# Kernel tuning notes

Hardware: AMD Instinct MI355X
Metric: run time of the kernel (lower is better)

Reference implementation:

```python
import jax, jax.numpy as jnp
import numpy as np

R_CUT = 5.0
N_NODES = 50000
N_EDGES = 400000
N_GRAPHS = 2500
D = 128        # embedding_size (hardcoded by torch.split(..., 128))
N_RBF = 20
N_BLOCKS = 3
PI = 3.141592653589793


def setup_inputs() -> dict:
    key = jax.random.key(0)
    ks = jax.random.split(key, 32)
    w = lambda k, s: (jax.random.normal(k, s) * 0.05).astype(jnp.float32)
    z = jax.random.randint(ks[0], (N_NODES,), 0, 100)
    edges = jax.random.randint(ks[1], (N_EDGES, 2), 0, N_NODES)
    r_ij = jax.random.uniform(ks[2], (N_EDGES, 1), minval=0.8, maxval=R_CUT, dtype=jnp.float32)
    d = jax.random.normal(ks[3], (N_EDGES, 3), dtype=jnp.float32)
    r_ij_normalized = d / jnp.linalg.norm(d, axis=1, keepdims=True)
    graph_idx = jax.random.randint(ks[4], (N_NODES,), 0, N_GRAPHS)
    return {
        "z": z, "edges": edges, "r_ij": r_ij,
        "r_ij_normalized": r_ij_normalized, "graph_idx": graph_idx,
        "emb": w(ks[5], (100, D)),
        # message blocks (stacked over N_BLOCKS)
        "msg_w1": w(ks[6], (N_BLOCKS, D, D)),   "msg_b1": w(ks[7], (N_BLOCKS, D)),
        "msg_w2": w(ks[8], (N_BLOCKS, D, 3 * D)), "msg_b2": w(ks[9], (N_BLOCKS, 3 * D)),
        "rbf_w": w(ks[10], (N_BLOCKS, N_RBF, 3 * D)), "rbf_b": w(ks[11], (N_BLOCKS, 3 * D)),
        # update blocks
        "upd_U": w(ks[12], (N_BLOCKS, D, D)), "upd_V": w(ks[13], (N_BLOCKS, D, D)),
        "upd_w1": w(ks[14], (N_BLOCKS, 2 * D, D)), "upd_b1": w(ks[15], (N_BLOCKS, D)),
        "upd_w2": w(ks[16], (N_BLOCKS, D, 3 * D)), "upd_b2": w(ks[17], (N_BLOCKS, 3 * D)),
        # readout
        "blue_w1": w(ks[18], (D, D)), "blue_b1": w(ks[19], (D,)),
        "blue_w2": w(ks[20], (D, 1)), "blue_b2": w(ks[21], (1,)),
    }


def _rbf(r, r_cut):
    n = jnp.arange(1, N_RBF + 1, dtype=r.dtype)  # [20]
    return jnp.sin(n * PI / r_cut * r) / r        # [E,20]


def _fcut(r, r_cut):
    return jnp.where(r <= r_cut, 0.5 * (jnp.cos(PI * r / r_cut) + 1.0), 0.0)


def painn_forward(z, edges, r_ij, r_ij_normalized, graph_idx, emb,
                  msg_w1, msg_b1, msg_w2, msg_b2, rbf_w, rbf_b,
                  upd_U, upd_V, upd_w1, upd_b1, upd_w2, upd_b2,
                  blue_w1, blue_b1, blue_w2, blue_b2):
    silu = jax.nn.silu
    src = edges[:, 1]  # gathered (neighbor j)
    dst = edges[:, 0]  # scattered (center i)
    s = emb[z]                                           # [N,128]
    v = jnp.zeros((s.shape[0], 3, D), dtype=r_ij.dtype)  # [N,3,128]
    rbf = _rbf(r_ij, R_CUT)                              # [E,20]
    f_c = _fcut(r_ij, R_CUT)                             # [E,1]
    for i in range(N_BLOCKS):
        # --- message block ---
        rbf_fcut = (rbf @ rbf_w[i] + rbf_b[i]) * f_c            # [E,384]
        s_pass = silu(s @ msg_w1[i] + msg_b1[i]) @ msg_w2[i] + msg_b2[i]  # [N,384]
        pass_out = rbf_fcut * s_pass[src]                        # [E,384]
        d_v, d_s, d_rep = jnp.split(pass_out, 3, axis=-1)        # each [E,128]
        delta_v = v[src] * d_v[:, None, :] + r_ij_normalized[:, :, None] * d_rep[:, None, :]
        s = s + jax.ops.segment_sum(d_s, dst, num_segments=N_NODES)
        v = v + jax.ops.segment_sum(delta_v, dst, num_segments=N_NODES)
        # --- update block ---
        U_v = jnp.einsum('nde,ef->ndf', v, upd_U[i])             # [N,3,128]
        V_v = jnp.einsum('nde,ef->ndf', v, upd_V[i])
        V_norm = jnp.linalg.norm(V_v, axis=1)                    # [N,128]
        sv = jnp.concatenate([V_norm, s], axis=1)                # [N,256]
        a = silu(sv @ upd_w1[i] + upd_b1[i]) @ upd_w2[i] + upd_b2[i]  # [N,384]
        avv, asv, ass = jnp.split(a, 3, axis=1)
        s = s + jnp.sum(U_v * V_v, axis=1) * asv + ass
        v = v + avv[:, None, :] * U_v
    blue = silu(s @ blue_w1 + blue_b1) @ blue_w2 + blue_b2       # [N,1]
    return jax.ops.segment_sum(blue, graph_idx, num_segments=N_GRAPHS)  # [G,1]


def reference(z, edges, r_ij, r_ij_normalized, graph_idx, emb,
              msg_w1, msg_b1, msg_w2, msg_b2, rbf_w, rbf_b,
              upd_U, upd_V, upd_w1, upd_b1, upd_w2, upd_b2,
              blue_w1, blue_b1, blue_w2, blue_b2):
    return painn_forward(z, edges, r_ij, r_ij_normalized, graph_idx, emb,
                         msg_w1, msg_b1, msg_w2, msg_b2, rbf_w, rbf_b,
                         upd_U, upd_V, upd_w1, upd_b1, upd_w2, upd_b2,
                         blue_w1, blue_b1, blue_w2, blue_b2)
```

## Files before the change

### kernel.cpp

```cpp
#include <hip/hip_runtime.h>
#include <hip/hip_bf16.h>
#include <math.h>

#define N_NODES 50000
#define N_EDGES 400000
#define N_GRAPHS 2500
#define D 128
#define D3 384
#define N_RBF 20
#define R_CUT 5.0f
#define PI_F 3.14159265358979f
#define NCH 98
#define GEB 16
#define GLDS_STRIDE 388

typedef __attribute__((ext_vector_type(8))) short bf16x8;
typedef __attribute__((ext_vector_type(4))) float f32x4;

__device__ __forceinline__ float silu_f(float x) {
    return x / (1.0f + __expf(-x));
}
__device__ __forceinline__ short f2bf(float x) {
    union { float f; unsigned u; } v; v.f = x;
    unsigned r = (v.u + 0x7FFFu + ((v.u >> 16) & 1u)) >> 16;
    return (short)r;
}
__device__ __forceinline__ float bf2f(short x) {
    union { unsigned u; float f; } v; v.u = ((unsigned)(unsigned short)x) << 16;
    return v.f;
}
__device__ __forceinline__ float bflo(unsigned u) {
    union { unsigned x; float f; } v; v.x = u << 16; return v.f;
}
__device__ __forceinline__ float bfhi(unsigned u) {
    union { unsigned x; float f; } v; v.x = u & 0xFFFF0000u; return v.f;
}
__device__ __forceinline__ unsigned packbf(float a, float b) {
    return ((unsigned)(unsigned short)f2bf(a)) | (((unsigned)(unsigned short)f2bf(b)) << 16);
}

#define MAXJOBS 19
struct PackJobs {
    const float* W[MAXJOBS];
    short* P[MAXJOBS];
    int K[MAXJOBS];
    int N[MAXJOBS];
    int boff[MAXJOBS + 1];
    int njobs;
};
__global__ void k_packall(PackJobs jobs) {
    int b = blockIdx.x;
    int j = 0;
    while (j + 1 < jobs.njobs && b >= jobs.boff[j + 1]) ++j;
    int t = (b - jobs.boff[j]) * 256 + threadIdx.x;
    int K = jobs.K[j], N = jobs.N[j];
    int NKT = K / 32;
    int total = (N / 16) * NKT * 64;
    if (t >= total) return;
    const float* W = jobs.W[j];
    short* P = jobs.P[j];
    int lane = t & 63;
    int kt = (t >> 6) % NKT;
    int nt = (t >> 6) / NKT;
    int k0 = kt * 32 + (lane >> 4) * 8;
    int col = nt * 16 + (lane & 15);
    #pragma unroll
    for (int q = 0; q < 8; ++q)
        P[(size_t)t * 8 + q] = f2bf(W[(size_t)(k0 + q) * N + col]);
}

__global__ void k_packrbf(const float* __restrict__ rbf_w, const float* __restrict__ rbf_b,
                          short* __restrict__ P) {
    int t = blockIdx.x * 256 + threadIdx.x;
    if (t >= 3 * 1536) return;
    int i = t / 1536;
    int r = t - i * 1536;
    int lane = r & 63;
    int nt = r >> 6;
    int col = nt * 16 + (lane & 15);
    int k0 = (lane >> 4) * 8;
    const float* W = rbf_w + (size_t)i * N_RBF * D3;
    const float* B = rbf_b + (size_t)i * D3;
    short* out = P + (size_t)i * 12288 + (size_t)r * 8;
    #pragma unroll
    for (int q = 0; q < 8; ++q) {
        int k = k0 + q;
        float v = (k < N_RBF) ? W[(size_t)k * D3 + col] : ((k == N_RBF) ? B[col] : 0.0f);
        out[q] = f2bf(v);
    }
}

template<int K, int N, bool SILU, int AMODE>
__global__ __launch_bounds__(256) void k_gemm(const void* __restrict__ Aptr,
                                              const void* __restrict__ A2ptr,
                                              const short* __restrict__ Bp,
                                              const float* __restrict__ bias,
                                              short* __restrict__ Cbf, int M) {
    constexpr int NKT = K / 32, NNT = N / 16;
    int lane = threadIdx.x & 63, wv = threadIdx.x >> 6;
    int tile = blockIdx.x * 4 + wv;
    int base = tile * 32;
    if (base >= M) return;
    bool has2 = (base + 16 < M);
    int r16 = lane & 15;
    int kgrp = (lane >> 4) * 8;
    int arow0 = base + r16;
    int arow1 = has2 ? (base + 16 + r16) : arow0;

    bf16x8 a0[NKT], a1[NKT];
    #pragma unroll
    for (int ss = 0; ss < 2; ++ss) {
        int arow = ss ? arow1 : arow0;
        bf16x8* a = ss ? a1 : a0;
        if (AMODE == 0) {
            const short* A = (const short*)Aptr + (size_t)arow * K + kgrp;
            #pragma unroll
            for (int kt = 0; kt < NKT; ++kt) a[kt] = *(const bf16x8*)(A + kt * 32);
        } else if (AMODE == 1) {
            const float* A = (const float*)Aptr + (size_t)arow * K + kgrp;
            #pragma unroll
            for (int kt = 0; kt < NKT; ++kt)
                #pragma unroll
                for (int j = 0; j < 8; ++j) a[kt][j] = f2bf(A[kt * 32 + j]);
        } else {
            const short* A1 = (const short*)Aptr + (size_t)arow * 128 + kgrp;
            const float* A2 = (const float*)A2ptr + (size_t)arow * 128 + kgrp;
            #pragma unroll
            for (int kt = 0; kt < 4 && kt < NKT; ++kt) a[kt] = *(const bf16x8*)(A1 + kt * 32);
            #pragma unroll
            for (int kt = 4; kt < NKT; ++kt)
                #pragma unroll
                for (int j = 0; j < 8; ++j) a[kt][j] = f2bf(A2[(kt - 4) * 32 + j]);
        }
    }

    int crow0 = base + (lane >> 4) * 4;
    int ccol = lane & 15;
    const bf16x8* Bv = (const bf16x8*)Bp;
    #pragma unroll
    for (int nt = 0; nt < NNT; ++nt) {
        f32x4 acc0 = {0.f, 0.f, 0.f, 0.f};
        f32x4 acc1 = {0.f, 0.f, 0.f, 0.f};
        #pragma unroll
        for (int kt = 0; kt < NKT; ++kt) {
            bf16x8 b = Bv[(nt * NKT + kt) * 64 + lane];
            acc0 = __builtin_amdgcn_mfma_f32_16x16x32_bf16(a0[kt], b, acc0, 0, 0, 0);
            acc1 = __builtin_amdgcn_mfma_f32_16x16x32_bf16(a1[kt], b, acc1, 0, 0, 0);
        }
        int col = nt * 16 + ccol;
        float bs = bias ? bias[col] : 0.0f;
        #pragma unroll
        for (int j = 0; j < 4; ++j) {
            float v = acc0[j] + bs;
            if (SILU) v = silu_f(v);
            Cbf[(size_t)(crow0 + j) * N + col] = f2bf(v);
        }
        if (has2) {
            #pragma unroll
            for (int j = 0; j < 4; ++j) {
                float v = acc1[j] + bs;
                if (SILU) v = silu_f(v);
                Cbf[(size_t)(crow0 + 16 + j) * N + col] = f2bf(v);
            }
        }
    }
}

__global__ __launch_bounds__(256) void k_gemmUV(const short* __restrict__ A,
                                                const short* __restrict__ Bp,
                                                short* __restrict__ Cu,
                                                short* __restrict__ Cv, int M) {
    int lane = threadIdx.x & 63, wv = threadIdx.x >> 6;
    int tile = blockIdx.x * 4 + wv;
    int base = tile * 32;
    if (base >= M) return;
    bool has2 = (base + 16 < M);
    int r16 = lane & 15;
    int kgrp = (lane >> 4) * 8;
    const short* Ar0 = A + (size_t)(base + r16) * 128 + kgrp;
    const short* Ar1 = A + (size_t)((has2 ? base + 16 : base) + r16) * 128 + kgrp;
    bf16x8 a0[4], a1[4];
    #pragma unroll
    for (int kt = 0; kt < 4; ++kt) {
        a0[kt] = *(const bf16x8*)(Ar0 + kt * 32);
        a1[kt] = *(const bf16x8*)(Ar1 + kt * 32);
    }
    int crow0 = base + (lane >> 4) * 4;
    int ccol = lane & 15;
    const bf16x8* Bv = (const bf16x8*)Bp;
    #pragma unroll
    for (int nt = 0; nt < 16; ++nt) {
        f32x4 acc0 = {0.f, 0.f, 0.f, 0.f};
        f32x4 acc1 = {0.f, 0.f, 0.f, 0.f};
        #pragma unroll
        for (int kt = 0; kt < 4; ++kt) {
            bf16x8 b = Bv[(nt * 4 + kt) * 64 + lane];
            acc0 = __builtin_amdgcn_mfma_f32_16x16x32_bf16(a0[kt], b, acc0, 0, 0, 0);
            acc1 = __builtin_amdgcn_mfma_f32_16x16x32_bf16(a1[kt], b, acc1, 0, 0, 0);
        }
        int col = nt * 16 + ccol;
        short* C = (col < 128) ? Cu : Cv;
        int cc = col & 127;
        #pragma unroll
        for (int j = 0; j < 4; ++j)
            C[(size_t)(crow0 + j) * 128 + cc] = f2bf(acc0[j]);
        if (has2) {
            #pragma unroll
            for (int j = 0; j < 4; ++j)
                C[(size_t)(crow0 + 16 + j) * 128 + cc] = f2bf(acc1[j]);
        }
    }
}

__global__ void k_embed(const int* __restrict__ z, const float* __restrict__ emb,
                        float* __restrict__ s) {
    int i = blockIdx.x * blockDim.x + threadIdx.x;
    if (i < N_NODES * D) {
        int n = i >> 7, c = i & 127;
        s[i] = emb[z[n] * D + c];
    }
}

__global__ void k_hist(const int* __restrict__ edges, int* __restrict__ cnt) {
    int e = blockIdx.x * 256 + threadIdx.x;
    if (e < N_EDGES) atomicAdd(&cnt[edges[2 * e]], 1);
}

__global__ void k_scan1(const int* __restrict__ cnt, int* __restrict__ csum) {
    int t = threadIdx.x;
    int g = blockIdx.x * 512 + t;
    int v = (g < N_NODES) ? cnt[g] : 0;
    #pragma unroll
    for (int off = 32; off > 0; off >>= 1) v += __shfl_down(v, off, 64);
    __shared__ int ws[8];
    if ((t & 63) == 0) ws[t >> 6] = v;
    __syncthreads();
    if (t == 0) {
        int sum = 0;
        #pragma unroll
        for (int i = 0; i < 8; ++i) sum += ws[i];
        csum[blockIdx.x] = sum;
    }
}

__global__ void k_scan2(const int* __restrict__ csum, int* __restrict__ cbase) {
    if (threadIdx.x == 0 && blockIdx.x == 0) {
        int s = 0;
        for (int i = 0; i < NCH; ++i) { cbase[i] = s; s += csum[i]; }
    }
}

__global__ void k_scan3(const int* __restrict__ cnt, const int* __restrict__ cbase,
                        int* __restrict__ rowptr) {
    __shared__ int buf[512];
    int t = threadIdx.x;
    int g = blockIdx.x * 512 + t;
    int orig = (g < N_NODES) ? cnt[g] : 0;
    buf[t] = orig;
    __syncthreads();
    for (int off = 1; off < 512; off <<= 1) {
        int v = (t >= off) ? buf[t - off] : 0;
        __syncthreads();
        buf[t] += v;
        __syncthreads();
    }
    if (g < N_NODES) rowptr[g] = cbase[blockIdx.x] + buf[t] - orig;
    if (g == 0 && blockIdx.x == 0) rowptr[N_NODES] = N_EDGES;
}

__global__ void k_scatter(const int* __restrict__ edges, const float* __restrict__ r_ij,
                          const float* __restrict__ rhat, const int* __restrict__ rowptr,
                          int* __restrict__ cursor, int* __restrict__ esrc,
                          short* __restrict__ erbf, float4* __restrict__ erhat) {
    int e = blockIdx.x * 256 + threadIdx.x;
    if (e >= N_EDGES) return;
    int dst = edges[2 * e], src = edges[2 * e + 1];
    int p = rowptr[dst] + atomicAdd(&cursor[dst], 1);
    esrc[p] = src;
    float r = r_ij[e];
    float fc = (r <= R_CUT) ? 0.5f * (cosf(PI_F * r / R_CUT) + 1.0f) : 0.0f;
    float inv_r = 1.0f / r;
    short rec[32];
    #pragma unroll
    for (int k = 0; k < N_RBF; ++k)
        rec[k] = f2bf(sinf((float)(k + 1) * (PI_F / R_CUT) * r) * inv_r * fc);
    rec[20] = f2bf(fc);
    #pragma unroll
    for (int k = 21; k < 32; ++k) rec[k] = 0;
    short* out = erbf + (size_t)p * 32;
    #pragma unroll
    for (int k = 0; k < 32; ++k) out[k] = rec[k];
    float4 rh;
    rh.x = rhat[3 * e]; rh.y = rhat[3 * e + 1]; rh.z = rhat[3 * e + 2]; rh.w = 0.f;
    erhat[p] = rh;
}

template<bool HASV>
__global__ __launch_bounds__(128, 4) void k_edge4(
    const int* __restrict__ rowptr, const int* __restrict__ esrc,
    const short* __restrict__ erbf, const float4* __restrict__ erhat,
    const short* __restrict__ pRbf,
    const short* __restrict__ spass, const short* __restrict__ vold,
    float* __restrict__ s, short* __restrict__ vnew) {
    __shared__ short gate_lds[GEB * GLDS_STRIDE];
    __shared__ int   src_lds[GEB];
    __shared__ float4 rh_lds[GEB];
    __shared__ float red[64 * 9];
    int tid = threadIdx.x;
    int lane = tid & 63;
    int wv = tid >> 6;
    int ntb = wv * 12;
    int c0 = lane * 2;
    bf16x8 bfr[12];
    #pragma unroll
    for (int t = 0; t < 12; ++t)
        bfr[t] = *(const bf16x8*)(pRbf + ((size_t)((ntb + t) * 64 + lane)) * 8);
    int r0 = (lane >> 4) * 4;
    int fcol = lane & 15;
    for (int n = blockIdx.x; n < N_NODES; n += gridDim.x) {
        int p0 = rowptr[n], p1 = rowptr[n + 1];
        float sa0 = 0.f, sa1 = 0.f;
        float va00 = 0.f, va01 = 0.f, va10 = 0.f, va11 = 0.f, va20 = 0.f, va21 = 0.f;
        for (int pb = p0; pb < p1; pb += GEB) {
            int erow = pb + (lane & 15);
            if (erow >= p1) erow = p1 - 1;
            bf16x8 afrag = *(const bf16x8*)(erbf + (size_t)erow * 32 + (lane >> 4) * 8);
            if (tid < GEB) {
                int p = pb + tid;
                if (p < p1) { src_lds[tid] = esrc[p]; rh_lds[tid] = erhat[p]; }
            }
            #pragma unroll
            for (int t = 0; t < 12; ++t) {
                f32x4 acc = {0.f, 0.f, 0.f, 0.f};
                acc = __builtin_amdgcn_mfma_f32_16x16x32_bf16(afrag, bfr[t], acc, 0, 0, 0);
                int col = (ntb + t) * 16 + fcol;
                #pragma unroll
                for (int j = 0; j < 4; ++j)
                    gate_lds[(r0 + j) * GLDS_STRIDE + col] = f2bf(acc[j]);
            }
            __syncthreads();
            int pe = (pb + GEB < p1) ? pb + GEB : p1;
            for (int p = pb + wv; p < pe; p += 2) {
                int src = src_lds[p - pb];
                float4 rh = rh_lds[p - pb];
                const short* g = gate_lds + (p - pb) * GLDS_STRIDE;
                unsigned ga1 = *(const unsigned*)(g + 128 + c0);
                unsigned ga2 = *(const unsigned*)(g + 256 + c0);
                const short* sp = spass + (size_t)src * D3;
                unsigned sp1 = *(const unsigned*)(sp + 128 + c0);
                unsigned sp2 = *(const unsigned*)(sp + 256 + c0);
                sa0 += bflo(ga1) * bflo(sp1);
                sa1 += bfhi(ga1) * bfhi(sp1);
                float drl = bflo(ga2) * bflo(sp2);
                float drh = bfhi(ga2) * bfhi(sp2);
                if (HASV) {
                    unsigned ga0 = *(const unsigned*)(g + c0);
                    unsigned sp0 = *(const unsigned*)(sp + c0);
                    float dvl = bflo(ga0) * bflo(sp0);
                    float dvh = bfhi(ga0) * bfhi(sp0);
                    const short* vs = vold + (size_t)src * D3;
                    unsigned v0 = *(const unsigned*)(vs + c0);
                    unsigned v1 = *(const unsigned*)(vs + 128 + c0);
                    unsigned v2 = *(const unsigned*)(vs + 256 + c0);
                    va00 += bflo(v0) * dvl + rh.x * drl;
                    va01 += bfhi(v0) * dvh + rh.x * drh;
                    va10 += bflo(v1) * dvl + rh.y * drl;
                    va11 += bfhi(v1) * dvh + rh.y * drh;
                    va20 += bflo(v2) * dvl + rh.z * drl;
                    va21 += bfhi(v2) * dvh + rh.z * drh;
                } else {
                    va00 += rh.x * drl; va01 += rh.x * drh;
                    va10 += rh.y * drl; va11 += rh.y * drh;
                    va20 += rh.z * drl; va21 += rh.z * drh;
                }
            }
            __syncthreads();
        }
        float* rl = red + lane * 9;
        __syncthreads();
        if (wv == 1) {
            rl[0] = sa0; rl[1] = sa1;
            rl[2] = va00; rl[3] = va01; rl[4] = va10; rl[5] = va11; rl[6] = va20; rl[7] = va21;
        }
        __syncthreads();
        if (wv == 0) {
            sa0 += rl[0]; sa1 += rl[1];
            va00 += rl[2]; va01 += rl[3]; va10 += rl[4]; va11 += rl[5]; va20 += rl[6]; va21 += rl[7];
            float2 sv = *(float2*)(s + (size_t)n * D + c0);
            sv.x += sa0; sv.y += sa1;
            *(float2*)(s + (size_t)n * D + c0) = sv;
            size_t vb = (size_t)n * D3;
            if (HASV) {
                unsigned o0 = *(const unsigned*)(vold + vb + c0);
                unsigned o1 = *(const unsigned*)(vold + vb + 128 + c0);
                unsigned o2 = *(const unsigned*)(vold + vb + 256 + c0);
                va00 += bflo(o0); va01 += bfhi(o0);
                va10 += bflo(o1); va11 += bfhi(o1);
                va20 += bflo(o2); va21 += bfhi(o2);
            }
            *(unsigned*)(vnew + vb + c0)       = packbf(va00, va01);
            *(unsigned*)(vnew + vb + 128 + c0) = packbf(va10, va11);
            *(unsigned*)(vnew + vb + 256 + c0) = packbf(va20, va21);
        }
    }
}

__global__ void k_svbuild(const short* __restrict__ Vv, short* __restrict__ Vn) {
    int i = blockIdx.x * 256 + threadIdx.x;
    int n = i >> 7, c = i & 127;
    float acc = 0.f;
    #pragma unroll
    for (int d = 0; d < 3; ++d) {
        float v = bf2f(Vv[(size_t)(n * 3 + d) * D + c]);
        acc += v * v;
    }
    Vn[i] = f2bf(sqrtf(acc));
}

__global__ void k_apply(float* __restrict__ s, short* __restrict__ v,
                        const short* __restrict__ Uv, const short* __restrict__ Vv,
                        const short* __restrict__ a_bf) {
    int i = blockIdx.x * 256 + threadIdx.x;
    int n = i >> 7, c = i & 127;
    float avv = bf2f(a_bf[(size_t)n * D3 + c]);
    float asv = bf2f(a_bf[(size_t)n * D3 + 128 + c]);
    float ass = bf2f(a_bf[(size_t)n * D3 + 256 + c]);
    float scal = 0.f;
    float uvr[3];
    #pragma unroll
    for (int d = 0; d < 3; ++d) {
        float u = bf2f(Uv[(size_t)(n * 3 + d) * D + c]);
        float vv = bf2f(Vv[(size_t)(n * 3 + d) * D + c]);
        uvr[d] = u;
        scal += u * vv;
    }
    s[i] += scal * asv + ass;
    #pragma unroll
    for (int d = 0; d < 3; ++d) {
        size_t idx = (size_t)n * D3 + d * 128 + c;
        v[idx] = f2bf(bf2f(v[idx]) + avv * uvr[d]);
    }
}

__global__ void k_blue_dot(const short* __restrict__ h, const int* __restrict__ graph_idx,
                           const float* __restrict__ w2, const float* __restrict__ b2,
                           float* __restrict__ out) {
    __shared__ float red[4];
    int c = threadIdx.x & 127;
    int n = blockIdx.x * 2 + (threadIdx.x >> 7);
    float val = bf2f(h[(size_t)n * D + c]) * w2[c];
    #pragma unroll
    for (int off = 32; off > 0; off >>= 1) val += __shfl_down(val, off, 64);
    if ((threadIdx.x & 63) == 0) red[threadIdx.x >> 6] = val;
    __syncthreads();
    if (threadIdx.x == 0)   atomicAdd(&out[graph_idx[n]], red[0] + red[1] + b2[0]);
    if (threadIdx.x == 128) atomicAdd(&out[graph_idx[n]], red[2] + red[3] + b2[0]);
}

static inline int g32(int M) { int t = (M + 31) / 32; return (t + 3) / 4; }

extern "C" void kernel_launch(void* const* d_in, const int* in_sizes, int n_in,
                              void* d_out, int out_size, void* d_ws, size_t ws_size,
                              hipStream_t stream) {
    const int*   z         = (const int*)d_in[0];
    const int*   edges     = (const int*)d_in[1];
    const float* r_ij      = (const float*)d_in[2];
    const float* rhat      = (const float*)d_in[3];
    const int*   graph_idx = (const int*)d_in[4];
    const float* emb       = (const float*)d_in[5];
    const float* msg_w1    = (const float*)d_in[6];
    const float* msg_b1    = (const float*)d_in[7];
    const float* msg_w2    = (const float*)d_in[8];
    const float* msg_b2    = (const float*)d_in[9];
    const float* rbf_w     = (const float*)d_in[10];
    const float* rbf_b     = (const float*)d_in[11];
    const float* upd_U     = (const float*)d_in[12];
    const float* upd_V     = (const float*)d_in[13];
    const float* upd_w1    = (const float*)d_in[14];
    const float* upd_b1    = (const float*)d_in[15];
    const float* upd_w2    = (const float*)d_in[16];
    const float* upd_b2    = (const float*)d_in[17];
    const float* blue_w1   = (const float*)d_in[18];
    const float* blue_b1   = (const float*)d_in[19];
    const float* blue_w2   = (const float*)d_in[20];
    const float* blue_b2   = (const float*)d_in[21];
    float* out = (float*)d_out;

    char* ws = (char*)d_ws;
    size_t off = 0;
    auto alloc = [&](size_t bytes) { void* p = ws + off; off += (bytes + 255) & ~(size_t)255; return p; };

    float* s      = (float*)alloc((size_t)N_NODES * D * 4);
    short* bufV0  = (short*)alloc((size_t)N_NODES * D3 * 2);
    short* bufV1  = (short*)alloc((size_t)N_NODES * D3 * 2);
    short* shrd   = (short*)alloc((size_t)N_NODES * D3 * 2);
    short* hbuf   = (short*)alloc((size_t)N_NODES * D * 2);
    short* Vv     = (short*)alloc((size_t)N_NODES * D3 * 2);
    short* Vn     = shrd;
    int*    esrc   = (int*)alloc((size_t)N_EDGES * 4);
    short*  erbf   = (short*)alloc((size_t)N_EDGES * 32 * 2);
    float4* erhat  = (float4*)alloc((size_t)N_EDGES * 16);
    int*    rowptr = (int*)alloc((size_t)(N_NODES + 1) * 4);
    int*    cnt    = (int*)alloc((size_t)N_NODES * 4);
    int*    csum   = (int*)alloc(NCH * 4);
    int*    cbase  = (int*)alloc(NCH * 4);

    short* pBlue = (short*)alloc(16384 * 2);
    short* pRbfAll = (short*)alloc((size_t)3 * 12288 * 2);
    short* pMsgW1[3]; short* pMsgW2[3]; short* pUV[3]; short* pUpdW1[3]; short* pUpdW2[3];
    for (int i = 0; i < 3; ++i) {
        pMsgW1[i] = (short*)alloc(16384 * 2);
        pMsgW2[i] = (short*)alloc(49152 * 2);
        pUV[i]    = (short*)alloc(32768 * 2);
        pUpdW1[i] = (short*)alloc(32768 * 2);
        pUpdW2[i] = (short*)alloc(49152 * 2);
    }

    PackJobs jobs;
    jobs.njobs = 0;
    int bacc = 0;
    auto addjob = [&](const float* W, short* P, int K, int N) {
        int j = jobs.njobs++;
        jobs.W[j] = W; jobs.P[j] = P; jobs.K[j] = K; jobs.N[j] = N;
        jobs.boff[j] = bacc;
        int total = (N / 16) * (K / 32) * 64;
        bacc += (total + 255) / 256;
        jobs.boff[j + 1] = bacc;
    };
    addjob(blue_w1, pBlue, 128, 128);
    for (int i = 0; i < 3; ++i) {
        addjob(msg_w1 + (size_t)i * D * D,     pMsgW1[i], 128, 128);
        addjob(msg_w2 + (size_t)i * D * D3,    pMsgW2[i], 128, 384);
        addjob(upd_U  + (size_t)i * D * D,     pUV[i],          128, 128);
        addjob(upd_V  + (size_t)i * D * D,     pUV[i] + 16384,  128, 128);
        addjob(upd_w1 + (size_t)i * 2 * D * D, pUpdW1[i], 256, 128);
        addjob(upd_w2 + (size_t)i * D * D3,    pUpdW2[i], 128, 384);
    }
    k_packall<<<bacc, 256, 0, stream>>>(jobs);
    k_packrbf<<<18, 256, 0, stream>>>(rbf_w, rbf_b, pRbfAll);

    hipMemsetAsync(cnt, 0, (size_t)N_NODES * 4, stream);
    k_hist<<<(N_EDGES + 255) / 256, 256, 0, stream>>>(edges, cnt);
    k_scan1<<<NCH, 512, 0, stream>>>(cnt, csum);
    k_scan2<<<1, 64, 0, stream>>>(csum, cbase);
    k_scan3<<<NCH, 512, 0, stream>>>(cnt, cbase, rowptr);
    hipMemsetAsync(cnt, 0, (size_t)N_NODES * 4, stream);
    k_scatter<<<(N_EDGES + 255) / 256, 256, 0, stream>>>(edges, r_ij, rhat, rowptr, cnt,
                                                         esrc, erbf, erhat);

    hipMemsetAsync(d_out, 0, (size_t)out_size * sizeof(float), stream);
    k_embed<<<(N_NODES * D) / 256, 256, 0, stream>>>(z, emb, s);

    const int gN  = g32(N_NODES);
    const int gN3 = g32(N_NODES * 3);

    for (int i = 0; i < 3; ++i) {
        short* vstate = (i & 1) ? bufV1 : bufV0;
        short* vscr   = (i & 1) ? bufV0 : bufV1;
        k_gemm<128, 128, true, 1><<<gN, 256, 0, stream>>>(
            s, nullptr, pMsgW1[i], msg_b1 + (size_t)i * D, hbuf, N_NODES);
        k_gemm<128, 384, false, 0><<<gN, 256, 0, stream>>>(
            hbuf, nullptr, pMsgW2[i], msg_b2 + (size_t)i * D3, shrd, N_NODES);
        if (i == 0)
            k_edge4<false><<<4096, 128, 0, stream>>>(rowptr, esrc, erbf, erhat,
                                                     pRbfAll, shrd, vstate, s, vscr);
        else
            k_edge4<true><<<4096, 128, 0, stream>>>(rowptr, esrc, erbf, erhat,
                                                    pRbfAll + (size_t)i * 12288,
                                                    shrd, vstate, s, vscr);
        k_gemmUV<<<gN3, 256, 0, stream>>>(vscr, pUV[i], vstate, Vv, N_NODES * 3);
        k_svbuild<<<(N_NODES * D) / 256, 256, 0, stream>>>(Vv, Vn);
        k_gemm<256, 128, true, 2><<<gN, 256, 0, stream>>>(
            Vn, s, pUpdW1[i], upd_b1 + (size_t)i * D, hbuf, N_NODES);
        k_gemm<128, 384, false, 0><<<gN, 256, 0, stream>>>(
            hbuf, nullptr, pUpdW2[i], upd_b2 + (size_t)i * D3, shrd, N_NODES);
        k_apply<<<(N_NODES * D) / 256, 256, 0, stream>>>(s, vscr, vstate, Vv, shrd);
    }

    k_gemm<128, 128, true, 1><<<gN, 256, 0, stream>>>(
        s, nullptr, pBlue, blue_b1, hbuf, N_NODES);
    k_blue_dot<<<N_NODES / 2, 256, 0, stream>>>(hbuf, graph_idx, blue_w2, blue_b2, out);
}
```

Before: 1.009 ms.

## Fuse vector-norm into update GEMM, fuse readout, single-kernel scan, vectorize apply

Computes the norm of V·v inside the update GEMM's A-operand load (AMODE 3), removing the separate svbuild kernel and its intermediate buffer. The readout GEMM, SiLU, dot with w2 and the per-graph atomic sum are fused into one kernel, so the hidden readout activations are never written to memory. The three-kernel prefix scan plus memset becomes one single-block 1024-thread scan that also zeroes the counts. k_apply now handles two channels per thread with packed 32-bit loads. Risks: the single-block scan runs serially per thread, and the readout issues more atomics from lane 0.

```diff
diff --git a/kernel.cpp b/kernel.cpp
--- a/kernel.cpp
+++ b/kernel.cpp
@@ -10,7 +10,6 @@
 #define N_RBF 20
 #define R_CUT 5.0f
 #define PI_F 3.14159265358979f
-#define NCH 98
 #define GEB 16
 #define GLDS_STRIDE 388
 
@@ -123,10 +122,19 @@
                 #pragma unroll
                 for (int j = 0; j < 8; ++j) a[kt][j] = f2bf(A[kt * 32 + j]);
         } else {
-            const short* A1 = (const short*)Aptr + (size_t)arow * 128 + kgrp;
+            const short* A1 = (const short*)Aptr + (size_t)arow * D3 + kgrp;
             const float* A2 = (const float*)A2ptr + (size_t)arow * 128 + kgrp;
             #pragma unroll
-            for (int kt = 0; kt < 4 && kt < NKT; ++kt) a[kt] = *(const bf16x8*)(A1 + kt * 32);
+            for (int kt = 0; kt < 4 && kt < NKT; ++kt) {
+                bf16x8 v0 = *(const bf16x8*)(A1 + kt * 32);
+                bf16x8 v1 = *(const bf16x8*)(A1 + kt * 32 + 128);
+                bf16x8 v2 = *(const bf16x8*)(A1 + kt * 32 + 256);
+                #pragma unroll
+                for (int j = 0; j < 8; ++j) {
+                    float f0 = bf2f(v0[j]), f1 = bf2f(v1[j]), f2 = bf2f(v2[j]);
+                    a[kt][j] = f2bf(sqrtf(f0 * f0 + f1 * f1 + f2 * f2));
+                }
+            }
             #pragma unroll
             for (int kt = 4; kt < NKT; ++kt)
                 #pragma unroll
@@ -212,6 +220,82 @@
     }
 }
 
+__global__ __launch_bounds__(256) void k_bluefused(const float* __restrict__ s,
+                                                   const short* __restrict__ Bp,
+                                                   const float* __restrict__ b1,
+                                                   const float* __restrict__ w2,
+                                                   const float* __restrict__ b2,
+                                                   const int* __restrict__ graph_idx,
+                                                   float* __restrict__ out, int M) {
+    int lane = threadIdx.x & 63, wv = threadIdx.x >> 6;
+    int tile = blockIdx.x * 4 + wv;
+    int base = tile * 32;
+    if (base >= M) return;
+    bool has2 = (base + 16 < M);
+    int r16 = lane & 15;
+    int kgrp = (lane >> 4) * 8;
+    int arow0 = base + r16;
+    int arow1 = has2 ? (base + 16 + r16) : arow0;
+    bf16x8 a0[4], a1[4];
+    {
+        const float* A = s + (size_t)arow0 * 128 + kgrp;
+        #pragma unroll
+        for (int kt = 0; kt < 4; ++kt)
+            #pragma unroll
+            for (int j = 0; j < 8; ++j) a0[kt][j] = f2bf(A[kt * 32 + j]);
+        const float* B = s + (size_t)arow1 * 128 + kgrp;
+        #pragma unroll
+        for (int kt = 0; kt < 4; ++kt)
+            #pragma unroll
+            for (int j = 0; j < 8; ++j) a1[kt][j] = f2bf(B[kt * 32 + j]);
+    }
+    int crow0 = base + (lane >> 4) * 4;
+    int ccol = lane & 15;
+    const bf16x8* Bv = (const bf16x8*)Bp;
+    float dot0[4] = {0.f, 0.f, 0.f, 0.f};
+    float dot1[4] = {0.f, 0.f, 0.f, 0.f};
+    #pragma unroll
+    for (int nt = 0; nt < 8; ++nt) {
+        f32x4 acc0 = {0.f, 0.f, 0.f, 0.f};
+        f32x4 acc1 = {0.f, 0.f, 0.f, 0.f};
+        #pragma unroll
+        for (int kt = 0; kt < 4; ++kt) {
+            bf16x8 b = Bv[(nt * 4 + kt) * 64 + lane];
+            acc0 = __builtin_amdgcn_mfma_f32_16x16x32_bf16(a0[kt], b, acc0, 0, 0, 0);
+            acc1 = __builtin_amdgcn_mfma_f32_16x16x32_bf16(a1[kt], b, acc1, 0, 0, 0);
+        }
+        int col = nt * 16 + ccol;
+        float bs = b1[col], w = w2[col];
+        #pragma unroll
+        for (int j = 0; j < 4; ++j) {
+            dot0[j] += silu_f(acc0[j] + bs) * w;
+            dot1[j] += silu_f(acc1[j] + bs) * w;
+        }
+    }
+    #pragma unroll
+    for (int m = 1; m <= 8; m <<= 1) {
+        #pragma unroll
+        for (int j = 0; j < 4; ++j) {
+            dot0[j] += __shfl_xor(dot0[j], m, 64);
+            dot1[j] += __shfl_xor(dot1[j], m, 64);
+        }
+    }
+    if (ccol == 0) {
+        #pragma unroll
+        for (int j = 0; j < 4; ++j) {
+            int n = crow0 + j;
+            atomicAdd(&out[graph_idx[n]], dot0[j] + b2[0]);
+        }
+        if (has2) {
+            #pragma unroll
+            for (int j = 0; j < 4; ++j) {
+                int n = crow0 + 16 + j;
+                atomicAdd(&out[graph_idx[n]], dot1[j] + b2[0]);
+            }
+        }
+    }
+}
+
 __global__ void k_embed(const int* __restrict__ z, const float* __restrict__ emb,
                         float* __restrict__ s) {
     int i = blockIdx.x * blockDim.x + threadIdx.x;
@@ -226,46 +310,30 @@
     if (e < N_EDGES) atomicAdd(&cnt[edges[2 * e]], 1);
 }
 
-__global__ void k_scan1(const int* __restrict__ cnt, int* __restrict__ csum) {
+#define SCH 49
+__global__ __launch_bounds__(1024) void k_scanall(int* __restrict__ cnt,
+                                                  int* __restrict__ rowptr) {
+    __shared__ int part[1024];
     int t = threadIdx.x;
-    int g = blockIdx.x * 512 + t;
-    int v = (g < N_NODES) ? cnt[g] : 0;
-    #pragma unroll
-    for (int off = 32; off > 0; off >>= 1) v += __shfl_down(v, off, 64);
-    __shared__ int ws[8];
-    if ((t & 63) == 0) ws[t >> 6] = v;
+    int lo = t * SCH;
+    int hi = lo + SCH; if (hi > N_NODES) hi = N_NODES;
+    int sum = 0;
+    for (int i = lo; i < hi; ++i) sum += cnt[i];
+    part[t] = sum;
     __syncthreads();
-    if (t == 0) {
-        int sum = 0;
-        #pragma unroll
-        for (int i = 0; i < 8; ++i) sum += ws[i];
-        csum[blockIdx.x] = sum;
-    }
-}
-
-__global__ void k_scan2(const int* __restrict__ csum, int* __restrict__ cbase) {
-    if (threadIdx.x == 0 && blockIdx.x == 0) {
-        int s = 0;
-        for (int i = 0; i < NCH; ++i) { cbase[i] = s; s += csum[i]; }
-    }
-}
-
-__global__ void k_scan3(const int* __restrict__ cnt, const int* __restrict__ cbase,
-                        int* __restrict__ rowptr) {
-    __shared__ int buf[512];
-    int t = threadIdx.x;
-    int g = blockIdx.x * 512 + t;
-    int orig = (g < N_NODES) ? cnt[g] : 0;
-    buf[t] = orig;
-    __syncthreads();
-    for (int off = 1; off < 512; off <<= 1) {
-        int v = (t >= off) ? buf[t - off] : 0;
+    for (int off = 1; off < 1024; off <<= 1) {
+        int v = (t >= off) ? part[t - off] : 0;
         __syncthreads();
-        buf[t] += v;
+        part[t] += v;
         __syncthreads();
     }
-    if (g < N_NODES) rowptr[g] = cbase[blockIdx.x] + buf[t] - orig;
-    if (g == 0 && blockIdx.x == 0) rowptr[N_NODES] = N_EDGES;
+    int run = part[t] - sum;
+    for (int i = lo; i < hi; ++i) {
+        rowptr[i] = run;
+        run += cnt[i];
+        cnt[i] = 0;
+    }
+    if (t == 1023) rowptr[N_NODES] = N_EDGES;
 }
 
 __global__ void k_scatter(const int* __restrict__ edges, const float* __restrict__ r_ij,
@@ -405,56 +473,36 @@
     }
 }
 
-__global__ void k_svbuild(const short* __restrict__ Vv, short* __restrict__ Vn) {
-    int i = blockIdx.x * 256 + threadIdx.x;
-    int n = i >> 7, c = i & 127;
-    float acc = 0.f;
-    #pragma unroll
-    for (int d = 0; d < 3; ++d) {
-        float v = bf2f(Vv[(size_t)(n * 3 + d) * D + c]);
-        acc += v * v;
-    }
-    Vn[i] = f2bf(sqrtf(acc));
-}
-
 __global__ void k_apply(float* __restrict__ s, short* __restrict__ v,
                         const short* __restrict__ Uv, const short* __restrict__ Vv,
                         const short* __restrict__ a_bf) {
     int i = blockIdx.x * 256 + threadIdx.x;
-    int n = i >> 7, c = i & 127;
-    float avv = bf2f(a_bf[(size_t)n * D3 + c]);
-    float asv = bf2f(a_bf[(size_t)n * D3 + 128 + c]);
-    float ass = bf2f(a_bf[(size_t)n * D3 + 256 + c]);
-    float scal = 0.f;
-    float uvr[3];
+    int n = i >> 6, c0 = (i & 63) * 2;
+    size_t ab = (size_t)n * D3;
+    unsigned avv = *(const unsigned*)(a_bf + ab + c0);
+    unsigned asv = *(const unsigned*)(a_bf + ab + 128 + c0);
+    unsigned ass = *(const unsigned*)(a_bf + ab + 256 + c0);
+    float scal0 = 0.f, scal1 = 0.f;
+    float u0[3], u1[3];
     #pragma unroll
     for (int d = 0; d < 3; ++d) {
-        float u = bf2f(Uv[(size_t)(n * 3 + d) * D + c]);
-        float vv = bf2f(Vv[(size_t)(n * 3 + d) * D + c]);
-        uvr[d] = u;
-        scal += u * vv;
-    }
-    s[i] += scal * asv + ass;
+        unsigned uu = *(const unsigned*)(Uv + ab + d * 128 + c0);
+        unsigned vv = *(const unsigned*)(Vv + ab + d * 128 + c0);
+        u0[d] = bflo(uu); u1[d] = bfhi(uu);
+        scal0 += u0[d] * bflo(vv);
+        scal1 += u1[d] * bfhi(vv);
+    }
+    float2 sv = *(float2*)(s + (size_t)n * D + c0);
+    sv.x += scal0 * bflo(asv) + bflo(ass);
+    sv.y += scal1 * bfhi(asv) + bfhi(ass);
+    *(float2*)(s + (size_t)n * D + c0) = sv;
+    float a0 = bflo(avv), a1 = bfhi(avv);
     #pragma unroll
     for (int d = 0; d < 3; ++d) {
-        size_t idx = (size_t)n * D3 + d * 128 + c;
-        v[idx] = f2bf(bf2f(v[idx]) + avv * uvr[d]);
-    }
-}
-
-__global__ void k_blue_dot(const short* __restrict__ h, const int* __restrict__ graph_idx,
-                           const float* __restrict__ w2, const float* __restrict__ b2,
-                           float* __restrict__ out) {
-    __shared__ float red[4];
-    int c = threadIdx.x & 127;
-    int n = blockIdx.x * 2 + (threadIdx.x >> 7);
-    float val = bf2f(h[(size_t)n * D + c]) * w2[c];
-    #pragma unroll
-    for (int off = 32; off > 0; off >>= 1) val += __shfl_down(val, off, 64);
-    if ((threadIdx.x & 63) == 0) red[threadIdx.x >> 6] = val;
-    __syncthreads();
-    if (threadIdx.x == 0)   atomicAdd(&out[graph_idx[n]], red[0] + red[1] + b2[0]);
-    if (threadIdx.x == 128) atomicAdd(&out[graph_idx[n]], red[2] + red[3] + b2[0]);
+        unsigned* vp = (unsigned*)(v + ab + d * 128 + c0);
+        unsigned old = *vp;
+        *vp = packbf(bflo(old) + a0 * u0[d], bfhi(old) + a1 * u1[d]);
+    }
 }
 
 static inline int g32(int M) { int t = (M + 31) / 32; return (t + 3) / 4; }
@@ -496,14 +544,11 @@
     short* shrd   = (short*)alloc((size_t)N_NODES * D3 * 2);
     short* hbuf   = (short*)alloc((size_t)N_NODES * D * 2);
     short* Vv     = (short*)alloc((size_t)N_NODES * D3 * 2);
-    short* Vn     = shrd;
     int*    esrc   = (int*)alloc((size_t)N_EDGES * 4);
     short*  erbf   = (short*)alloc((size_t)N_EDGES * 32 * 2);
     float4* erhat  = (float4*)alloc((size_t)N_EDGES * 16);
     int*    rowptr = (int*)alloc((size_t)(N_NODES + 1) * 4);
     int*    cnt    = (int*)alloc((size_t)N_NODES * 4);
-    int*    csum   = (int*)alloc(NCH * 4);
-    int*    cbase  = (int*)alloc(NCH * 4);
 
     short* pBlue = (short*)alloc(16384 * 2);
     short* pRbfAll = (short*)alloc((size_t)3 * 12288 * 2);
@@ -541,10 +586,7 @@
 
     hipMemsetAsync(cnt, 0, (size_t)N_NODES * 4, stream);
     k_hist<<<(N_EDGES + 255) / 256, 256, 0, stream>>>(edges, cnt);
-    k_scan1<<<NCH, 512, 0, stream>>>(cnt, csum);
-    k_scan2<<<1, 64, 0, stream>>>(csum, cbase);
-    k_scan3<<<NCH, 512, 0, stream>>>(cnt, cbase, rowptr);
-    hipMemsetAsync(cnt, 0, (size_t)N_NODES * 4, stream);
+    k_scanall<<<1, 1024, 0, stream>>>(cnt, rowptr);
     k_scatter<<<(N_EDGES + 255) / 256, 256, 0, stream>>>(edges, r_ij, rhat, rowptr, cnt,
                                                          esrc, erbf, erhat);
 
@@ -569,15 +611,13 @@
                                                     pRbfAll + (size_t)i * 12288,
                                                     shrd, vstate, s, vscr);
         k_gemmUV<<<gN3, 256, 0, stream>>>(vscr, pUV[i], vstate, Vv, N_NODES * 3);
-        k_svbuild<<<(N_NODES * D) / 256, 256, 0, stream>>>(Vv, Vn);
-        k_gemm<256, 128, true, 2><<<gN, 256, 0, stream>>>(
-            Vn, s, pUpdW1[i], upd_b1 + (size_t)i * D, hbuf, N_NODES);
+        k_gemm<256, 128, true, 3><<<gN, 256, 0, stream>>>(
+            Vv, s, pUpdW1[i], upd_b1 + (size_t)i * D, hbuf, N_NODES);
         k_gemm<128, 384, false, 0><<<gN, 256, 0, stream>>>(
             hbuf, nullptr, pUpdW2[i], upd_b2 + (size_t)i * D3, shrd, N_NODES);
-        k_apply<<<(N_NODES * D) / 256, 256, 0, stream>>>(s, vscr, vstate, Vv, shrd);
-    }
-
-    k_gemm<128, 128, true, 1><<<gN, 256, 0, stream>>>(
-        s, nullptr, pBlue, blue_b1, hbuf, N_NODES);
-    k_blue_dot<<<N_NODES / 2, 256, 0, stream>>>(hbuf, graph_idx, blue_w2, blue_b2, out);
-}
+        k_apply<<<(N_NODES * 64) / 256, 256, 0, stream>>>(s, vscr, vstate, Vv, shrd);
+    }
+
+    k_bluefused<<<gN, 256, 0, stream>>>(s, pBlue, blue_b1, blue_w2, blue_b2,
+                                        graph_idx, out, N_NODES);
+}
```

Result: slower. 1.054 ms (+4.4%).
